# Kernel optimization log

Hardware: AMD Instinct MI355X
Metric: run time of the kernel (lower is better)

The kernel has to match this reference:

```python
import jax, jax.numpy as jnp
import numpy as np

B, T, N, FIN, FOUT, EDGE_DIM = 8, 16, 256, 32, 32, 16


def setup_inputs() -> dict:
    key = jax.random.key(0)
    ks = jax.random.split(key, 8)
    def xavier(k, shape):
        fan_in, fan_out = shape[0], shape[1]
        limit = float(np.sqrt(6.0 / (fan_in + fan_out)))
        return jax.random.uniform(k, shape, jnp.float32, -limit, limit)
    return {
        "x": jax.random.normal(ks[0], (B, T, N, FIN), jnp.float32),
        "adj": jax.random.uniform(ks[1], (N, N), jnp.float32),
        # edge_net: Linear(1, edge_dim) -> GELU -> Linear(edge_dim, Fin*Fout)
        "w1": xavier(ks[2], (1, EDGE_DIM)),
        "b1": jnp.zeros((EDGE_DIM,), jnp.float32),
        "w2": xavier(ks[3], (EDGE_DIM, FIN * FOUT)),
        "b2": jnp.zeros((FIN * FOUT,), jnp.float32),
        # node_lin: Linear(Fin, Fout)
        "node_w": xavier(ks[4], (FIN, FOUT)),
        "node_b": jnp.zeros((FOUT,), jnp.float32),
    }


def reference(x, adj, w1, b1, w2, b2, node_w, node_b):
    # edge-conditioned weights: (N, N, Fin, Fout)
    h = jax.nn.gelu(adj[:, :, None] * w1[0] + b1, approximate=False)  # (N,N,E)
    edge_w = (h @ w2 + b2).reshape(N, N, FIN, FOUT)
    # msg[b,t,i,j,:] = sum_f x[b,t,j,f] * edge_w[i,j,f,:]; agg = sum_j msg
    agg = jnp.einsum("btjf,ijfo->btio", x, edge_w)  # (B,T,N,Fout)
    y = jax.nn.gelu(x @ node_w + node_b + agg, approximate=False)
    return y
```

## Files before the change

### kernel.cpp

```cpp
#include <hip/hip_runtime.h>
#include <math.h>

#define NB    256
#define EDIM  16
#define FINN  32
#define FOUTN 32
#define BT    128
#define KKD   4096

typedef __attribute__((ext_vector_type(8))) short short8;
typedef __attribute__((ext_vector_type(4))) float floatx4;

#define MFMA16(a,b,c) __builtin_amdgcn_mfma_f32_16x16x32_bf16((a),(b),(c),0,0,0)

#define BARRIER() asm volatile("s_waitcnt lgkmcnt(0)\n\ts_barrier" ::: "memory")

__device__ __forceinline__ float gelu_f(float v) {
    return 0.5f * v * (1.0f + erff(v * 0.70710678118654752f));
}
__device__ __forceinline__ ushort f2bf(float x) {
    union { float f; unsigned u; } v; v.f = x;
    unsigned r = (v.u + 0x7FFFu + ((v.u >> 16) & 1u)) >> 16;
    return (ushort)r;
}
__device__ __forceinline__ float bf2f(ushort b) {
    union { unsigned u; float f; } v; v.u = ((unsigned)b) << 16; return v.f;
}

__global__ __launch_bounds__(256) void h_kernel(const float* __restrict__ adj,
                                                const float* __restrict__ w1,
                                                const float* __restrict__ b1,
                                                const float* __restrict__ w2,
                                                ushort* __restrict__ Hf,
                                                ushort* __restrict__ w2f) {
    int tid = threadIdx.x;
    if (blockIdx.x >= 128) {
        for (int s = 0; s < 2048; s += 256) {
            int slot = s + tid;
            int e = slot >> 7, r = slot & 127;
            int ot = r >> 6, lane = r & 63;
            int m = lane & 15, quad = lane >> 4;
            const float* src = w2 + (size_t)e * 1024 + (quad * 8) * 32 + ot * 16 + m;
            ushort tmp[8];
            #pragma unroll
            for (int i = 0; i < 8; ++i) tmp[i] = f2bf(src[i * 32]);
            *(int4*)(w2f + (size_t)slot * 8) = *(int4*)tmp;
        }
        return;
    }
    __shared__ float adjs[16][264];
    __shared__ float w1s[16], b1s[16];
    int it = blockIdx.x & 15;
    int kq = blockIdx.x >> 4;
    if (tid < 16) { w1s[tid] = w1[tid]; b1s[tid] = b1[tid]; }
    #pragma unroll
    for (int q = 0; q < 4; ++q) {
        int u = q * 256 + tid;
        int row = u >> 6, c4 = u & 63;
        *(float4*)&adjs[row][c4 * 4] =
            ((const float4*)(adj + ((size_t)it * 16 + row) * 256))[c4];
    }
    __syncthreads();
    #pragma unroll
    for (int q = 0; q < 4; ++q) {
        int u = q * 256 + tid;
        int ks = kq * 16 + (u >> 6);
        int lane = u & 63;
        int m = lane & 15, quad = lane >> 4;
        int e = ks >> 3;
        int j0 = (ks & 7) * 32 + quad * 8;
        float w = w1s[e], b = b1s[e];
        ushort tmp[8];
        #pragma unroll
        for (int d = 0; d < 8; ++d)
            tmp[d] = f2bf(gelu_f(adjs[m][j0 + d] * w + b));
        *(int4*)(Hf + (((size_t)it * 128 + ks) * 64 + lane) * 8) = *(int4*)tmp;
    }
}

#define NCH  16
#define BSP  264
#define XBP  40

__global__ __launch_bounds__(256, 2) void fused_kernel(
        const float* __restrict__ x,      const ushort* __restrict__ w2f,
        const float* __restrict__ b2,     const float* __restrict__ node_w,
        const float* __restrict__ node_b, const ushort* __restrict__ Hf,
        float* __restrict__ out) {
    __shared__ ushort xb[NB][XBP];
    __shared__ ushort Bs[2][32][BSP];
    __shared__ ushort nwT[32][XBP];
    __shared__ float  Sp[8][32];
    __shared__ float  Sv[32];
    __shared__ float  bias2[32];

    int bt   = blockIdx.x;
    int iq   = blockIdx.y;
    int tid  = threadIdx.x;
    int wv   = tid >> 6;
    int lane = tid & 63;
    int m    = lane & 15;
    int quad = lane >> 4;
    int it   = iq * 4 + wv;
    int i0g  = it * 16;

    const ushort* Hlane = Hf + (size_t)it * 128 * 512 + lane * 8;
    const ushort* Wlane = w2f + (size_t)lane * 8;

    short8 areg[2][8];
    short8 wreg[2][2];

    #define ALOAD(dst, c)                                                     \
    {                                                                         \
        _Pragma("unroll")                                                     \
        for (int kk = 0; kk < 8; ++kk)                                        \
            dst[kk] = *(const short8*)(Hlane + ((c) * 8 + kk) * 512);         \
    }
    #define WLOADB(dst, e)                                                    \
    {                                                                         \
        dst[0] = *(const short8*)(Wlane + (size_t)(e) * 1024);                \
        dst[1] = *(const short8*)(Wlane + (size_t)(e) * 1024 + 512);          \
    }

    WLOADB(wreg[0], 0);

    const float4* xg = (const float4*)(x + (size_t)bt * NB * FINN);
    #pragma unroll
    for (int itr = 0; itr < 8; ++itr) {
        int idx4 = itr * 256 + tid;
        float4 v = xg[idx4];
        int j = idx4 >> 3, f = (idx4 & 7) * 4;
        uint2 p;
        p.x = (unsigned)f2bf(v.x) | ((unsigned)f2bf(v.y) << 16);
        p.y = (unsigned)f2bf(v.z) | ((unsigned)f2bf(v.w) << 16);
        *(uint2*)&xb[j][f] = p;
    }
    {
        float4 v = ((const float4*)node_w)[tid];
        int f = tid >> 3, o = (tid & 7) * 4;
        nwT[o + 0][f] = f2bf(v.x); nwT[o + 1][f] = f2bf(v.y);
        nwT[o + 2][f] = f2bf(v.z); nwT[o + 3][f] = f2bf(v.w);
    }
    __syncthreads();

    {
        int f = tid & 31, grp = tid >> 5;
        float s = 0.f;
        for (int j = grp * 32; j < grp * 32 + 32; ++j) s += bf2f(xb[j][f]);
        Sp[grp][f] = s;
    }

    short8 afr[4];
    #pragma unroll
    for (int t = 0; t < 4; ++t)
        afr[t] = *(short8*)&xb[(wv * 4 + t) * 16 + m][quad * 8];

    __syncthreads();
    if (tid < 32) {
        float s = 0.f;
        #pragma unroll
        for (int g = 0; g < 8; ++g) s += Sp[g][tid];
        Sv[tid] = s;
    }

    floatx4 acc[2] = {};

    #define PRODUCE(buf, w)                                                   \
    {                                                                         \
        _Pragma("unroll")                                                     \
        for (int t = 0; t < 4; ++t) {                                         \
            floatx4 z = {0.f, 0.f, 0.f, 0.f};                                 \
            floatx4 d0 = MFMA16(afr[t], w[0], z);                             \
            floatx4 d1 = MFMA16(afr[t], w[1], z);                             \
            int col = (wv * 4 + t) * 16 + quad * 4;                           \
            uint2 p0, p1;                                                     \
            p0.x = (unsigned)f2bf(d0[0]) | ((unsigned)f2bf(d0[1]) << 16);     \
            p0.y = (unsigned)f2bf(d0[2]) | ((unsigned)f2bf(d0[3]) << 16);     \
            p1.x = (unsigned)f2bf(d1[0]) | ((unsigned)f2bf(d1[1]) << 16);     \
            p1.y = (unsigned)f2bf(d1[2]) | ((unsigned)f2bf(d1[3]) << 16);     \
            *(uint2*)&Bs[buf][     m][col] = p0;                              \
            *(uint2*)&Bs[buf][16 + m][col] = p1;                              \
        }                                                                     \
    }
    #define GEMMC(buf, ar)                                                    \
    {                                                                         \
        _Pragma("unroll")                                                     \
        for (int kk = 0; kk < 8; ++kk) {                                      \
            short8 b0 = *(short8*)&Bs[buf][     m][kk * 32 + quad * 8];       \
            short8 b1 = *(short8*)&Bs[buf][16 + m][kk * 32 + quad * 8];       \
            acc[0] = MFMA16(ar[kk], b0, acc[0]);                              \
            acc[1] = MFMA16(ar[kk], b1, acc[1]);                              \
        }                                                                     \
    }

    #pragma unroll
    for (int c = 0; c < NCH; ++c) {
        ALOAD(areg[c & 1], c);
        if (c < NCH - 1) WLOADB(wreg[(c + 1) & 1], c + 1);
        PRODUCE(c & 1, wreg[c & 1]);
        if (c > 0) {
            GEMMC((c - 1) & 1, areg[(c - 1) & 1]);
        } else if (tid < 32) {
            float bb = node_b[tid];
            #pragma unroll
            for (int f = 0; f < FINN; ++f) bb += Sv[f] * b2[f * FOUTN + tid];
            bias2[tid] = bb;
        }
        BARRIER();
    }
    GEMMC((NCH - 1) & 1, areg[(NCH - 1) & 1]);

    {
        short8 xa = *(short8*)&xb[i0g + m][quad * 8];
        #pragma unroll
        for (int tn = 0; tn < 2; ++tn) {
            short8 nb = *(short8*)&nwT[tn * 16 + m][quad * 8];
            acc[tn] = MFMA16(xa, nb, acc[tn]);
        }
    }
    #pragma unroll
    for (int tn = 0; tn < 2; ++tn) {
        int o = tn * 16 + m;
        float bz = bias2[o];
        #pragma unroll
        for (int r = 0; r < 4; ++r) {
            int row = i0g + quad * 4 + r;
            out[((size_t)bt * NB + row) * FOUTN + o] = gelu_f(acc[tn][r] + bz);
        }
    }
}

extern "C" void kernel_launch(void* const* d_in, const int* in_sizes, int n_in,
                              void* d_out, int out_size, void* d_ws, size_t ws_size,
                              hipStream_t stream) {
    const float* x      = (const float*)d_in[0];
    const float* adj    = (const float*)d_in[1];
    const float* w1     = (const float*)d_in[2];
    const float* b1     = (const float*)d_in[3];
    const float* w2     = (const float*)d_in[4];
    const float* b2     = (const float*)d_in[5];
    const float* node_w = (const float*)d_in[6];
    const float* node_b = (const float*)d_in[7];
    float* out = (float*)d_out;

    ushort* Hf  = (ushort*)d_ws;
    ushort* w2f = Hf + (size_t)NB * KKD;

    hipLaunchKernelGGL(h_kernel, dim3(129), dim3(256), 0, stream,
                       adj, w1, b1, w2, Hf, w2f);
    hipLaunchKernelGGL(fused_kernel, dim3(BT, 4), dim3(256), 0, stream,
                       x, w2f, b2, node_w, node_b, Hf, out);
}
```

Before: 96.40 us.

## Precompute x·W2 products globally and stream them into LDS via direct loads

```diff
diff --git a/kernel.cpp b/kernel.cpp
--- a/kernel.cpp
+++ b/kernel.cpp
@@ -6,14 +6,12 @@
 #define FINN  32
 #define FOUTN 32
 #define BT    128
-#define KKD   4096
+
 
 typedef __attribute__((ext_vector_type(8))) short short8;
 typedef __attribute__((ext_vector_type(4))) float floatx4;
 
 #define MFMA16(a,b,c) __builtin_amdgcn_mfma_f32_16x16x32_bf16((a),(b),(c),0,0,0)
-
-#define BARRIER() asm volatile("s_waitcnt lgkmcnt(0)\n\ts_barrier" ::: "memory")
 
 __device__ __forceinline__ float gelu_f(float v) {
     return 0.5f * v * (1.0f + erff(v * 0.70710678118654752f));
@@ -23,211 +21,215 @@
     unsigned r = (v.u + 0x7FFFu + ((v.u >> 16) & 1u)) >> 16;
     return (ushort)r;
 }
-__device__ __forceinline__ float bf2f(ushort b) {
-    union { unsigned u; float f; } v; v.u = ((unsigned)b) << 16; return v.f;
-}
-
-__global__ __launch_bounds__(256) void h_kernel(const float* __restrict__ adj,
-                                                const float* __restrict__ w1,
-                                                const float* __restrict__ b1,
-                                                const float* __restrict__ w2,
-                                                ushort* __restrict__ Hf,
-                                                ushort* __restrict__ w2f) {
+__device__ __forceinline__ uint2 pack4(floatx4 d) {
+    uint2 p;
+    p.x = (unsigned)f2bf(d[0]) | ((unsigned)f2bf(d[1]) << 16);
+    p.y = (unsigned)f2bf(d[2]) | ((unsigned)f2bf(d[3]) << 16);
+    return p;
+}
+
+typedef __attribute__((address_space(1))) void gvoid_t;
+typedef __attribute__((address_space(3))) void lvoid_t;
+__device__ __forceinline__ void gload_lds16(const void* g, void* l) {
+    __builtin_amdgcn_global_load_lds((gvoid_t*)g, (lvoid_t*)l, 16, 0, 0);
+}
+
+__global__ __launch_bounds__(256) void prep_kernel(
+        const float* __restrict__ x,   const float* __restrict__ adj,
+        const float* __restrict__ w1,  const float* __restrict__ b1,
+        const float* __restrict__ w2,  const float* __restrict__ b2,
+        const float* __restrict__ node_w, const float* __restrict__ node_b,
+        ushort* __restrict__ Hf, ushort* __restrict__ y2f,
+        float* __restrict__ bias2g, ushort* __restrict__ nwf) {
+    int bid = blockIdx.x;
     int tid = threadIdx.x;
-    if (blockIdx.x >= 128) {
-        for (int s = 0; s < 2048; s += 256) {
-            int slot = s + tid;
-            int e = slot >> 7, r = slot & 127;
-            int ot = r >> 6, lane = r & 63;
+    __shared__ float adjs[16][264];
+    __shared__ float w1s[16], b1s[16];
+    __shared__ float Sp[8][32];
+    __shared__ float Svs[32];
+
+    if (bid < 1024) {
+        int bt = bid >> 3, ep = bid & 7;
+        int wv = tid >> 6, lane = tid & 63, m = lane & 15, quad = lane >> 4;
+        short8 xf[4];
+        #pragma unroll
+        for (int t = 0; t < 4; ++t) {
+            int jt = wv * 4 + t;
+            const float* xs = x + ((size_t)bt * NB + jt * 16 + m) * FINN + quad * 8;
+            float4 lo = *(const float4*)xs;
+            float4 hi = *(const float4*)(xs + 4);
+            ushort tmp[8];
+            tmp[0]=f2bf(lo.x); tmp[1]=f2bf(lo.y); tmp[2]=f2bf(lo.z); tmp[3]=f2bf(lo.w);
+            tmp[4]=f2bf(hi.x); tmp[5]=f2bf(hi.y); tmp[6]=f2bf(hi.z); tmp[7]=f2bf(hi.w);
+            xf[t] = *(short8*)tmp;
+        }
+        #pragma unroll
+        for (int ee = 0; ee < 2; ++ee) {
+            int e = ep * 2 + ee;
+            short8 wf[2];
+            #pragma unroll
+            for (int ot = 0; ot < 2; ++ot) {
+                ushort tmp[8];
+                #pragma unroll
+                for (int d = 0; d < 8; ++d)
+                    tmp[d] = f2bf(w2[(size_t)e * 1024 + (quad * 8 + d) * 32 + ot * 16 + m]);
+                wf[ot] = *(short8*)tmp;
+            }
+            #pragma unroll
+            for (int t = 0; t < 4; ++t) {
+                int jt = wv * 4 + t;
+                floatx4 z = {0.f, 0.f, 0.f, 0.f};
+                floatx4 d0 = MFMA16(xf[t], wf[0], z);
+                floatx4 d1 = MFMA16(xf[t], wf[1], z);
+                int ks = e * 8 + (jt >> 1);
+                int qp = (jt & 1) * 2 + (quad >> 1);
+                int dp = (quad & 1) * 4;
+                size_t base = ((size_t)bt * 128 + ks) * 1024;
+                *(uint2*)(y2f + base +       (qp * 16 + m) * 8 + dp) = pack4(d0);
+                *(uint2*)(y2f + base + 512 + (qp * 16 + m) * 8 + dp) = pack4(d1);
+            }
+        }
+        if (ep == 0) {
+            int f = tid & 31, grp = tid >> 5;
+            float s = 0.f;
+            for (int j = grp; j < NB; j += 8)
+                s += x[((size_t)bt * NB + j) * FINN + f];
+            Sp[grp][f] = s;
+            __syncthreads();
+            if (tid < 32) {
+                float s2 = 0.f;
+                #pragma unroll
+                for (int g = 0; g < 8; ++g) s2 += Sp[g][tid];
+                Svs[tid] = s2;
+            }
+            __syncthreads();
+            if (tid < 32) {
+                float bb = node_b[tid];
+                #pragma unroll
+                for (int f2 = 0; f2 < FINN; ++f2)
+                    bb += Svs[f2] * b2[f2 * FOUTN + tid];
+                bias2g[bt * 32 + tid] = bb;
+            }
+        }
+        return;
+    }
+    if (bid < 1152) {
+        int hb = bid - 1024;
+        int it = hb & 15;
+        int kq = hb >> 4;
+        if (tid < 16) { w1s[tid] = w1[tid]; b1s[tid] = b1[tid]; }
+        #pragma unroll
+        for (int q = 0; q < 4; ++q) {
+            int u = q * 256 + tid;
+            int row = u >> 6, c4 = u & 63;
+            *(float4*)&adjs[row][c4 * 4] =
+                ((const float4*)(adj + ((size_t)it * 16 + row) * 256))[c4];
+        }
+        __syncthreads();
+        #pragma unroll
+        for (int q = 0; q < 4; ++q) {
+            int u = q * 256 + tid;
+            int ks = kq * 16 + (u >> 6);
+            int lane = u & 63;
             int m = lane & 15, quad = lane >> 4;
-            const float* src = w2 + (size_t)e * 1024 + (quad * 8) * 32 + ot * 16 + m;
+            int e = ks >> 3;
+            int j0 = (ks & 7) * 32 + quad * 8;
+            float w = w1s[e], b = b1s[e];
             ushort tmp[8];
             #pragma unroll
-            for (int i = 0; i < 8; ++i) tmp[i] = f2bf(src[i * 32]);
-            *(int4*)(w2f + (size_t)slot * 8) = *(int4*)tmp;
+            for (int d = 0; d < 8; ++d)
+                tmp[d] = f2bf(gelu_f(adjs[m][j0 + d] * w + b));
+            *(int4*)(Hf + (((size_t)it * 128 + ks) * 64 + lane) * 8) = *(int4*)tmp;
         }
         return;
     }
-    __shared__ float adjs[16][264];
-    __shared__ float w1s[16], b1s[16];
-    int it = blockIdx.x & 15;
-    int kq = blockIdx.x >> 4;
-    if (tid < 16) { w1s[tid] = w1[tid]; b1s[tid] = b1[tid]; }
-    #pragma unroll
-    for (int q = 0; q < 4; ++q) {
-        int u = q * 256 + tid;
-        int row = u >> 6, c4 = u & 63;
-        *(float4*)&adjs[row][c4 * 4] =
-            ((const float4*)(adj + ((size_t)it * 16 + row) * 256))[c4];
-    }
-    __syncthreads();
-    #pragma unroll
-    for (int q = 0; q < 4; ++q) {
-        int u = q * 256 + tid;
-        int ks = kq * 16 + (u >> 6);
-        int lane = u & 63;
-        int m = lane & 15, quad = lane >> 4;
-        int e = ks >> 3;
-        int j0 = (ks & 7) * 32 + quad * 8;
-        float w = w1s[e], b = b1s[e];
+    if (tid < 128) {
+        int ot = tid >> 6, lane = tid & 63, m = lane & 15, q = lane >> 4;
         ushort tmp[8];
         #pragma unroll
         for (int d = 0; d < 8; ++d)
-            tmp[d] = f2bf(gelu_f(adjs[m][j0 + d] * w + b));
-        *(int4*)(Hf + (((size_t)it * 128 + ks) * 64 + lane) * 8) = *(int4*)tmp;
-    }
-}
-
-#define NCH  16
-#define BSP  264
-#define XBP  40
-
-__global__ __launch_bounds__(256, 2) void fused_kernel(
-        const float* __restrict__ x,      const ushort* __restrict__ w2f,
-        const float* __restrict__ b2,     const float* __restrict__ node_w,
-        const float* __restrict__ node_b, const ushort* __restrict__ Hf,
-        float* __restrict__ out) {
-    __shared__ ushort xb[NB][XBP];
-    __shared__ ushort Bs[2][32][BSP];
-    __shared__ ushort nwT[32][XBP];
-    __shared__ float  Sp[8][32];
-    __shared__ float  Sv[32];
-    __shared__ float  bias2[32];
+            tmp[d] = f2bf(node_w[(q * 8 + d) * 32 + ot * 16 + m]);
+        *(int4*)(nwf + tid * 8) = *(int4*)tmp;
+    }
+}
+
+__global__ __launch_bounds__(512, 2) void fused_kernel(
+        const float* __restrict__ x,      const ushort* __restrict__ Hf,
+        const ushort* __restrict__ y2f,   const float* __restrict__ bias2g,
+        const ushort* __restrict__ nwf,   float* __restrict__ out) {
+    __shared__ ushort Bsl[2][16][2][64][8];
 
     int bt   = blockIdx.x;
-    int iq   = blockIdx.y;
+    int iq2  = blockIdx.y;
     int tid  = threadIdx.x;
     int wv   = tid >> 6;
     int lane = tid & 63;
     int m    = lane & 15;
     int quad = lane >> 4;
-    int it   = iq * 4 + wv;
+    int it   = iq2 * 8 + wv;
     int i0g  = it * 16;
 
-    const ushort* Hlane = Hf + (size_t)it * 128 * 512 + lane * 8;
-    const ushort* Wlane = w2f + (size_t)lane * 8;
-
-    short8 areg[2][8];
-    short8 wreg[2][2];
-
-    #define ALOAD(dst, c)                                                     \
+    const ushort* Hlane = Hf + (size_t)it * 65536 + lane * 8;
+    const ushort* y2bt  = y2f + (size_t)bt * 131072;
+
+    floatx4 acc[2] = {};
+
+    #define STAGE(buf, c)                                                     \
+    {                                                                         \
+        const ushort* s_ = y2bt + (size_t)(c) * 16384;                        \
+        ushort* d_ = &Bsl[buf][0][0][0][0];                                   \
+        _Pragma("unroll")                                                     \
+        for (int s = 0; s < 4; ++s)                                           \
+            gload_lds16(s_ + s * 4096 + tid * 8, d_ + s * 4096 + tid * 8);    \
+    }
+    #define GEMMC(buf, c)                                                     \
     {                                                                         \
         _Pragma("unroll")                                                     \
-        for (int kk = 0; kk < 8; ++kk)                                        \
-            dst[kk] = *(const short8*)(Hlane + ((c) * 8 + kk) * 512);         \
-    }
-    #define WLOADB(dst, e)                                                    \
-    {                                                                         \
-        dst[0] = *(const short8*)(Wlane + (size_t)(e) * 1024);                \
-        dst[1] = *(const short8*)(Wlane + (size_t)(e) * 1024 + 512);          \
-    }
-
-    WLOADB(wreg[0], 0);
-
-    const float4* xg = (const float4*)(x + (size_t)bt * NB * FINN);
+        for (int kk = 0; kk < 16; ++kk) {                                     \
+            short8 a  = *(const short8*)(Hlane + ((c) * 16 + kk) * 512);      \
+            short8 b0 = *(const short8*)&Bsl[buf][kk][0][lane][0];            \
+            short8 b1 = *(const short8*)&Bsl[buf][kk][1][lane][0];            \
+            acc[0] = MFMA16(a, b0, acc[0]);                                   \
+            acc[1] = MFMA16(a, b1, acc[1]);                                   \
+        }                                                                     \
+    }
+
+    STAGE(0, 0);
+    __syncthreads();
     #pragma unroll
-    for (int itr = 0; itr < 8; ++itr) {
-        int idx4 = itr * 256 + tid;
-        float4 v = xg[idx4];
-        int j = idx4 >> 3, f = (idx4 & 7) * 4;
-        uint2 p;
-        p.x = (unsigned)f2bf(v.x) | ((unsigned)f2bf(v.y) << 16);
-        p.y = (unsigned)f2bf(v.z) | ((unsigned)f2bf(v.w) << 16);
-        *(uint2*)&xb[j][f] = p;
-    }
+    for (int c = 0; c < 8; ++c) {
+        if (c < 7) STAGE((c + 1) & 1, c + 1);
+        GEMMC(c & 1, c);
+        __syncthreads();
+    }
+
+    short8 xa;
     {
-        float4 v = ((const float4*)node_w)[tid];
-        int f = tid >> 3, o = (tid & 7) * 4;
-        nwT[o + 0][f] = f2bf(v.x); nwT[o + 1][f] = f2bf(v.y);
-        nwT[o + 2][f] = f2bf(v.z); nwT[o + 3][f] = f2bf(v.w);
-    }
-    __syncthreads();
-
-    {
-        int f = tid & 31, grp = tid >> 5;
-        float s = 0.f;
-        for (int j = grp * 32; j < grp * 32 + 32; ++j) s += bf2f(xb[j][f]);
-        Sp[grp][f] = s;
-    }
-
-    short8 afr[4];
+        const float* xs = x + ((size_t)bt * NB + i0g + m) * FINN + quad * 8;
+        float4 lo = *(const float4*)xs;
+        float4 hi = *(const float4*)(xs + 4);
+        ushort tmp[8];
+        tmp[0]=f2bf(lo.x); tmp[1]=f2bf(lo.y); tmp[2]=f2bf(lo.z); tmp[3]=f2bf(lo.w);
+        tmp[4]=f2bf(hi.x); tmp[5]=f2bf(hi.y); tmp[6]=f2bf(hi.z); tmp[7]=f2bf(hi.w);
+        xa = *(short8*)tmp;
+    }
     #pragma unroll
-    for (int t = 0; t < 4; ++t)
-        afr[t] = *(short8*)&xb[(wv * 4 + t) * 16 + m][quad * 8];
-
-    __syncthreads();
-    if (tid < 32) {
-        float s = 0.f;
-        #pragma unroll
-        for (int g = 0; g < 8; ++g) s += Sp[g][tid];
-        Sv[tid] = s;
-    }
-
-    floatx4 acc[2] = {};
-
-    #define PRODUCE(buf, w)                                                   \
-    {                                                                         \
-        _Pragma("unroll")                                                     \
-        for (int t = 0; t < 4; ++t) {                                         \
-            floatx4 z = {0.f, 0.f, 0.f, 0.f};                                 \
-            floatx4 d0 = MFMA16(afr[t], w[0], z);                             \
-            floatx4 d1 = MFMA16(afr[t], w[1], z);                             \
-            int col = (wv * 4 + t) * 16 + quad * 4;                           \
-            uint2 p0, p1;                                                     \
-            p0.x = (unsigned)f2bf(d0[0]) | ((unsigned)f2bf(d0[1]) << 16);     \
-            p0.y = (unsigned)f2bf(d0[2]) | ((unsigned)f2bf(d0[3]) << 16);     \
-            p1.x = (unsigned)f2bf(d1[0]) | ((unsigned)f2bf(d1[1]) << 16);     \
-            p1.y = (unsigned)f2bf(d1[2]) | ((unsigned)f2bf(d1[3]) << 16);     \
-            *(uint2*)&Bs[buf][     m][col] = p0;                              \
-            *(uint2*)&Bs[buf][16 + m][col] = p1;                              \
-        }                                                                     \
-    }
-    #define GEMMC(buf, ar)                                                    \
-    {                                                                         \
-        _Pragma("unroll")                                                     \
-        for (int kk = 0; kk < 8; ++kk) {                                      \
-            short8 b0 = *(short8*)&Bs[buf][     m][kk * 32 + quad * 8];       \
-            short8 b1 = *(short8*)&Bs[buf][16 + m][kk * 32 + quad * 8];       \
-            acc[0] = MFMA16(ar[kk], b0, acc[0]);                              \
-            acc[1] = MFMA16(ar[kk], b1, acc[1]);                              \
-        }                                                                     \
-    }
-
-    #pragma unroll
-    for (int c = 0; c < NCH; ++c) {
-        ALOAD(areg[c & 1], c);
-        if (c < NCH - 1) WLOADB(wreg[(c + 1) & 1], c + 1);
-        PRODUCE(c & 1, wreg[c & 1]);
-        if (c > 0) {
-            GEMMC((c - 1) & 1, areg[(c - 1) & 1]);
-        } else if (tid < 32) {
-            float bb = node_b[tid];
-            #pragma unroll
-            for (int f = 0; f < FINN; ++f) bb += Sv[f] * b2[f * FOUTN + tid];
-            bias2[tid] = bb;
-        }
-        BARRIER();
-    }
-    GEMMC((NCH - 1) & 1, areg[(NCH - 1) & 1]);
-
-    {
-        short8 xa = *(short8*)&xb[i0g + m][quad * 8];
-        #pragma unroll
-        for (int tn = 0; tn < 2; ++tn) {
-            short8 nb = *(short8*)&nwT[tn * 16 + m][quad * 8];
-            acc[tn] = MFMA16(xa, nb, acc[tn]);
-        }
+    for (int tn = 0; tn < 2; ++tn) {
+        short8 nb = *(const short8*)(nwf + (tn * 64 + lane) * 8);
+        acc[tn] = MFMA16(xa, nb, acc[tn]);
     }
     #pragma unroll
     for (int tn = 0; tn < 2; ++tn) {
         int o = tn * 16 + m;
-        float bz = bias2[o];
+        float bz = bias2g[bt * 32 + o];
         #pragma unroll
         for (int r = 0; r < 4; ++r) {
             int row = i0g + quad * 4 + r;
             out[((size_t)bt * NB + row) * FOUTN + o] = gelu_f(acc[tn][r] + bz);
         }
     }
+    #undef STAGE
+    #undef GEMMC
 }
 
 extern "C" void kernel_launch(void* const* d_in, const int* in_sizes, int n_in,
@@ -243,11 +245,14 @@
     const float* node_b = (const float*)d_in[7];
     float* out = (float*)d_out;
 
-    ushort* Hf  = (ushort*)d_ws;
-    ushort* w2f = Hf + (size_t)NB * KKD;
-
-    hipLaunchKernelGGL(h_kernel, dim3(129), dim3(256), 0, stream,
-                       adj, w1, b1, w2, Hf, w2f);
-    hipLaunchKernelGGL(fused_kernel, dim3(BT, 4), dim3(256), 0, stream,
-                       x, w2f, b2, node_w, node_b, Hf, out);
-}
+    ushort* Hf     = (ushort*)d_ws;
+    ushort* y2f    = Hf + (size_t)(1 << 20);
+    float*  bias2g = (float*)(y2f + (size_t)(1 << 24));
+    ushort* nwf    = (ushort*)(bias2g + 128 * 32);
+
+    hipLaunchKernelGGL(prep_kernel, dim3(1153), dim3(256), 0, stream,
+                       x, adj, w1, b1, w2, b2, node_w, node_b,
+                       Hf, y2f, bias2g, nwf);
+    hipLaunchKernelGGL(fused_kernel, dim3(BT, 2), dim3(512), 0, stream,
+                       x, Hf, y2f, bias2g, nwf, out);
+}
```

After: 111.5 us. +15.7%, slower.
